# Kernel optimization log

Hardware: AMD Instinct MI355X
Metric: run time of the kernel (lower is better)

The kernel has to match this reference:

```python
import jax, jax.numpy as jnp
import numpy as np

B, N, C = 2, 4096, 256
H = 8          # num heads
D = C // H     # head dim = 32
SR = 2         # spatial reduction ratio
HID = 1024     # mixffn hidden = 4*C
EPS = 1e-5


def layernorm(x, g, b):
    mu = jnp.mean(x, axis=-1, keepdims=True)
    var = jnp.mean(jnp.square(x - mu), axis=-1, keepdims=True)
    return (x - mu) * jax.lax.rsqrt(var + EPS) * g + b


def conv2d(x, w, b, stride, pad, groups=1):
    out = jax.lax.conv_general_dilated(
        x, w, (stride, stride), [(pad, pad), (pad, pad)],
        dimension_numbers=("NCHW", "OIHW", "NCHW"), feature_group_count=groups)
    return out + b[None, :, None, None]


def setup_inputs() -> dict:
    key = jax.random.key(0)
    ks = jax.random.split(key, 20)
    s = lambda k, shape, scale=0.02: jax.random.normal(k, shape, jnp.float32) * scale
    return {
        "x": jax.random.normal(ks[0], (B, N, C), jnp.float32),
        "h": 64, "w": 64,
        "ln1_g": jnp.ones((C,), jnp.float32), "ln1_b": jnp.zeros((C,), jnp.float32),
        "q_w": s(ks[1], (C, C)),
        "kv_w": s(ks[2], (2 * C, C)),
        "sr_w": s(ks[3], (C, C, SR, SR)), "sr_b": jnp.zeros((C,), jnp.float32),
        "srn_g": jnp.ones((C,), jnp.float32), "srn_b": jnp.zeros((C,), jnp.float32),
        "proj_w": s(ks[4], (C, C)), "proj_b": jnp.zeros((C,), jnp.float32),
        "ln2_g": jnp.ones((C,), jnp.float32), "ln2_b": jnp.zeros((C,), jnp.float32),
        "fc1_w": s(ks[5], (HID, C)), "fc1_b": jnp.zeros((HID,), jnp.float32),
        "pe_w": s(ks[6], (HID, 1, 3, 3)), "pe_b": jnp.zeros((HID,), jnp.float32),
        "fc2_w": s(ks[7], (C, HID)), "fc2_b": jnp.zeros((C,), jnp.float32),
    }


def reference(x, h, w, ln1_g, ln1_b, q_w, kv_w, sr_w, sr_b, srn_g, srn_b,
              proj_w, proj_b, ln2_g, ln2_b, fc1_w, fc1_b, pe_w, pe_b, fc2_w, fc2_b):
    b_, n_, c_ = x.shape
    # ---- attention branch ----
    xn = layernorm(x, ln1_g, ln1_b)
    q = jnp.einsum("bnc,oc->bno", xn, q_w).reshape(b_, n_, H, D).transpose(0, 2, 1, 3)  # [B,H,N,D]
    # spatial-reduction of KV
    x_kv = xn.reshape(b_, h, w, c_).transpose(0, 3, 1, 2)              # [B,C,h,w]
    x_kv = conv2d(x_kv, sr_w, sr_b, stride=SR, pad=0)                  # [B,C,h/SR,w/SR]
    nkv = (h // SR) * (w // SR)
    x_kv = x_kv.reshape(b_, c_, nkv).transpose(0, 2, 1)                # [B,Nkv,C]
    x_kv = layernorm(x_kv, srn_g, srn_b)
    kv = jnp.einsum("bnc,oc->bno", x_kv, kv_w).reshape(b_, nkv, 2, H, D)
    k = kv[:, :, 0].transpose(0, 2, 1, 3)                              # [B,H,Nkv,D]
    v = kv[:, :, 1].transpose(0, 2, 1, 3)
    scale = D ** -0.5
    att = jax.nn.softmax(jnp.einsum("bhxd,bhyd->bhxy", q, k) * scale, axis=-1)
    o = jnp.einsum("bhxy,bhyd->bhxd", att, v)                          # [B,H,N,D]
    o = o.transpose(0, 2, 1, 3).reshape(b_, n_, c_)
    o = jnp.einsum("bnc,oc->bno", o, proj_w) + proj_b
    x = x + o
    # ---- Mix-FFN branch ----
    xn2 = layernorm(x, ln2_g, ln2_b)
    xf = xn2.reshape(b_, h, w, c_).transpose(0, 3, 1, 2)               # [B,C,h,w]
    xf = jnp.einsum("bchw,oc->bohw", xf, fc1_w) + fc1_b[None, :, None, None]
    xf = conv2d(xf, pe_w, pe_b, stride=1, pad=1, groups=HID)           # depthwise 3x3
    xf = jax.nn.gelu(xf, approximate=False)
    xf = jnp.einsum("bchw,oc->bohw", xf, fc2_w) + fc2_b[None, :, None, None]
    xf = xf.transpose(0, 2, 3, 1).reshape(b_, n_, c_)
    return x + xf
```

## Files before the change

### kernel.cpp

```cpp
#include <hip/hip_runtime.h>
#include <math.h>

constexpr int BB   = 2;
constexpr int NN   = 4096;
constexpr int CCH  = 256;
constexpr int NH   = 8;
constexpr int HD   = 32;
constexpr int GW   = 64;
constexpr int NKV  = 1024;
constexpr int HIDN = 1024;
constexpr float EPSF = 1e-5f;

typedef short  bf16x8 __attribute__((ext_vector_type(8)));
typedef short  bf16x4 __attribute__((ext_vector_type(4)));
typedef float  f32x4  __attribute__((ext_vector_type(4)));

__device__ __forceinline__ short f2bf(float f) {
    unsigned int u = __float_as_uint(f);
    unsigned int r = (u + 0x7FFFu + ((u >> 16) & 1u)) >> 16;
    return (short)r;
}
__device__ __forceinline__ float bf2f(short s) {
    return __uint_as_float(((unsigned int)(unsigned short)s) << 16);
}
__device__ __forceinline__ unsigned int cvtpk_bf16(float a, float b) {
    unsigned int r;
    asm("v_cvt_pk_bf16_f32 %0, %1, %2" : "=v"(r) : "v"(a), "v"(b));
    return r;
}
__device__ __forceinline__ void gl16(const void* g, void* l) {
    __builtin_amdgcn_global_load_lds(
        (const __attribute__((address_space(1))) void*)g,
        (__attribute__((address_space(3))) void*)l, 16, 0, 0);
}

__global__ __launch_bounds__(256) void prep_kernel(const float* __restrict__ q_w,
                                                   const float* __restrict__ kv_w,
                                                   const float* __restrict__ proj_w,
                                                   const float* __restrict__ fc1_w,
                                                   const float* __restrict__ fc2_w,
                                                   const float* __restrict__ sr_w,
                                                   short* qwb, short* kvwb, short* pjwb,
                                                   short* f1wb, short* f2wb, short* srwb,
                                                   const float* __restrict__ x,
                                                   const float* __restrict__ ln1_g,
                                                   const float* __restrict__ ln1_b,
                                                   short* __restrict__ xn) {
    __shared__ float pa[4], pb[4];
    int t = threadIdx.x;
    if (blockIdx.x < 4096) {
        int i = blockIdx.x * 256 + t;
        if (i < 65536) { qwb[i] = f2bf(q_w[i] * 0.17677669529663687f); return; }
        i -= 65536;
        if (i < 131072) { kvwb[i] = f2bf(kv_w[i]); return; }
        i -= 131072;
        if (i < 65536) { pjwb[i] = f2bf(proj_w[i]); return; }
        i -= 65536;
        if (i < 262144) { f1wb[i] = f2bf(fc1_w[i]); return; }
        i -= 262144;
        if (i < 262144) { f2wb[i] = f2bf(fc2_w[i]); return; }
        i -= 262144;
        {
            int o = i >> 10, rem = i & 1023, c = rem >> 2, q = rem & 3;
            srwb[o * 1024 + q * 256 + c] = f2bf(sr_w[i]);
        }
        return;
    }
    int row = blockIdx.x - 4096;
    float v = x[row * CCH + t];
    float a = v, b = v * v;
#pragma unroll
    for (int off = 32; off > 0; off >>= 1) {
        a += __shfl_xor(a, off);
        b += __shfl_xor(b, off);
    }
    int w = t >> 6;
    if ((t & 63) == 0) { pa[w] = a; pb[w] = b; }
    __syncthreads();
    a = pa[0] + pa[1] + pa[2] + pa[3];
    b = pb[0] + pb[1] + pb[2] + pb[3];
    float mu = a * (1.0f / CCH);
    float var = b * (1.0f / CCH) - mu * mu;
    float rs = rsqrtf(var + EPSF);
    xn[row * CCH + t] = f2bf((v - mu) * rs * ln1_g[t] + ln1_b[t]);
}

template <bool INBF>
__global__ __launch_bounds__(256) void ln_wave(const void* __restrict__ in,
                                               const float* __restrict__ g,
                                               const float* __restrict__ bta,
                                               short* __restrict__ out) {
    int t = threadIdx.x;
    int w = t >> 6, lane = t & 63;
    int row = blockIdx.x * 4 + w;
    float v[4];
    if (INBF) {
        bf16x4 bv = *(const bf16x4*)&((const short*)in)[(size_t)row * CCH + lane * 4];
#pragma unroll
        for (int j = 0; j < 4; j++) v[j] = bf2f(bv[j]);
    } else {
        float4 fv = *(const float4*)&((const float*)in)[(size_t)row * CCH + lane * 4];
        v[0] = fv.x; v[1] = fv.y; v[2] = fv.z; v[3] = fv.w;
    }
    float a = v[0] + v[1] + v[2] + v[3];
    float b = v[0]*v[0] + v[1]*v[1] + v[2]*v[2] + v[3]*v[3];
#pragma unroll
    for (int off = 1; off < 64; off <<= 1) {
        a += __shfl_xor(a, off);
        b += __shfl_xor(b, off);
    }
    float mu = a * (1.0f / CCH);
    float var = b * (1.0f / CCH) - mu * mu;
    float rs = rsqrtf(var + EPSF);
    bf16x4 ov;
#pragma unroll
    for (int j = 0; j < 4; j++)
        ov[j] = f2bf((v[j] - mu) * rs * g[lane * 4 + j] + bta[lane * 4 + j]);
    *(bf16x4*)&out[(size_t)row * CCH + lane * 4] = ov;
}

template <bool OUTB, int RESMODE>
__device__ __forceinline__ void gemm64_body(const short* __restrict__ A,
                                            const short* __restrict__ W,
                                            const float* __restrict__ bias,
                                            const void* __restrict__ res,
                                            void* __restrict__ outp,
                                            int M, int O, int K, int bx, int by,
                                            short (*As0)[64], short (*Ws0)[64],
                                            short (*As1)[64], short (*Ws1)[64]) {
    int t = threadIdx.x;
    int m0 = by * 64, o0 = bx * 64;
    int w = t >> 6, lane = t & 63;
    int wm = (w >> 1) * 32, wn = (w & 1) * 32;
    int fr = lane & 15, fq = lane >> 4;
    int srow = lane >> 3;
    int sg   = (lane & 7) ^ srow;
    f32x4 acc[2][2];
#pragma unroll
    for (int mi = 0; mi < 2; mi++)
#pragma unroll
        for (int ni = 0; ni < 2; ni++)
            acc[mi][ni] = f32x4{0.f, 0.f, 0.f, 0.f};

    auto stage = [&](short (*Asb)[64], short (*Wsb)[64], int k0) {
#pragma unroll
        for (int r = 0; r < 2; r++) {
            int rowA = r * 32 + w * 8 + srow;
            gl16(&A[(size_t)(m0 + rowA) * K + k0 + sg * 8], &Asb[r * 32 + w * 8][0]);
            gl16(&W[(size_t)(o0 + rowA) * K + k0 + sg * 8], &Wsb[r * 32 + w * 8][0]);
        }
    };
    auto compute = [&](short (*Asb)[64], short (*Wsb)[64]) {
#pragma unroll
        for (int half = 0; half < 2; half++) {
            bf16x8 af[2], wf[2];
#pragma unroll
            for (int mi = 0; mi < 2; mi++) {
                int row = wm + mi * 16 + fr;
                af[mi] = *(const bf16x8*)&Asb[row][(((half << 2) | fq) ^ (row & 7)) * 8];
            }
#pragma unroll
            for (int ni = 0; ni < 2; ni++) {
                int row = wn + ni * 16 + fr;
                wf[ni] = *(const bf16x8*)&Wsb[row][(((half << 2) | fq) ^ (row & 7)) * 8];
            }
#pragma unroll
            for (int mi = 0; mi < 2; mi++)
#pragma unroll
                for (int ni = 0; ni < 2; ni++)
                    acc[mi][ni] = __builtin_amdgcn_mfma_f32_16x16x32_bf16(
                        af[mi], wf[ni], acc[mi][ni], 0, 0, 0);
        }
    };

    stage(As0, Ws0, 0);
    __syncthreads();
    for (int k0 = 0; k0 < K; k0 += 128) {
        if (k0 + 64 < K) stage(As1, Ws1, k0 + 64);
        compute(As0, Ws0);
        __syncthreads();
        if (k0 + 128 < K) stage(As0, Ws0, k0 + 128);
        if (k0 + 64 < K) compute(As1, Ws1);
        __syncthreads();
    }
#pragma unroll
    for (int mi = 0; mi < 2; mi++)
#pragma unroll
        for (int ni = 0; ni < 2; ni++)
#pragma unroll
            for (int r = 0; r < 4; r++) {
                int m = m0 + wm + mi * 16 + fq * 4 + r;
                int o = o0 + wn + ni * 16 + fr;
                float v = acc[mi][ni][r];
                if (bias) v += bias[o];
                if (RESMODE == 1) v += ((const float*)res)[(size_t)m * O + o];
                if (RESMODE == 2) v += bf2f(((const short*)res)[(size_t)m * O + o]);
                if (OUTB) ((short*)outp)[(size_t)m * O + o] = f2bf(v);
                else      ((float*)outp)[(size_t)m * O + o] = v;
            }
}

template <bool OUTB, int RESMODE>
__global__ __launch_bounds__(256, 4) void gemm64(const short* __restrict__ A,
                                                 const short* __restrict__ W,
                                                 const float* __restrict__ bias,
                                                 const void* __restrict__ res,
                                                 void* __restrict__ outp,
                                                 int M, int O, int K) {
    __shared__ short As0[64][64], Ws0[64][64];
    __shared__ short As1[64][64], Ws1[64][64];
    gemm64_body<OUTB, RESMODE>(A, W, bias, res, outp, M, O, K,
                               blockIdx.x, blockIdx.y, As0, Ws0, As1, Ws1);
}

__device__ __forceinline__ void sr_body(const short* __restrict__ xn,
                                        const short* __restrict__ Wsr,
                                        const float* __restrict__ sr_b,
                                        float* __restrict__ srtmp, int bx, int by,
                                        short (*As0)[64], short (*As1)[64],
                                        short (*Ws0)[64], short (*Ws1)[64]) {
    int t = threadIdx.x;
    int m0 = by * 32, o0 = bx * 64;
    int w = t >> 6, lane = t & 63;
    int wm = (w >> 1) * 16, wn = (w & 1) * 32;
    int fr = lane & 15, fq = lane >> 4;
    int srow = lane >> 3;
    int sg   = (lane & 7) ^ srow;
    int arow = w * 8 + srow;
    int p = m0 + arow;
    int b = p >> 10, pp = p & 1023, ii = pp >> 5, jj = pp & 31;
    int nbase = ii * 128 + jj * 2;
    size_t xbase = (size_t)(b * NN) * CCH;
    f32x4 acc[2];
    acc[0] = f32x4{0.f, 0.f, 0.f, 0.f};
    acc[1] = f32x4{0.f, 0.f, 0.f, 0.f};

    auto stage = [&](short (*Asb)[64], short (*Wsb)[64], int k0) {
        int q = k0 >> 8, c0 = k0 & 255;
        int n = nbase + (q >> 1) * 64 + (q & 1);
        gl16(&xn[xbase + (size_t)n * CCH + c0 + sg * 8], &Asb[w * 8][0]);
#pragma unroll
        for (int r = 0; r < 2; r++)
            gl16(&Wsr[(size_t)(o0 + r * 32 + w * 8 + srow) * 1024 + k0 + sg * 8],
                 &Wsb[r * 32 + w * 8][0]);
    };
    auto compute = [&](short (*Asb)[64], short (*Wsb)[64]) {
#pragma unroll
        for (int half = 0; half < 2; half++) {
            int cg = (half << 2) | fq;
            int rowa = wm + fr;
            bf16x8 af = *(const bf16x8*)&Asb[rowa][(cg ^ (rowa & 7)) * 8];
            bf16x8 wf[2];
#pragma unroll
            for (int ni = 0; ni < 2; ni++) {
                int row = wn + ni * 16 + fr;
                wf[ni] = *(const bf16x8*)&Wsb[row][(cg ^ (row & 7)) * 8];
            }
#pragma unroll
            for (int ni = 0; ni < 2; ni++)
                acc[ni] = __builtin_amdgcn_mfma_f32_16x16x32_bf16(
                    af, wf[ni], acc[ni], 0, 0, 0);
        }
    };

    stage(As0, Ws0, 0);
    __syncthreads();
    for (int k0 = 0; k0 < 1024; k0 += 128) {
        if (k0 + 64 < 1024) stage(As1, Ws1, k0 + 64);
        compute(As0, Ws0);
        __syncthreads();
        if (k0 + 128 < 1024) stage(As0, Ws0, k0 + 128);
        compute(As1, Ws1);
        __syncthreads();
    }
#pragma unroll
    for (int ni = 0; ni < 2; ni++)
#pragma unroll
        for (int r = 0; r < 4; r++) {
            int m = m0 + wm + fq * 4 + r;
            int o = o0 + wn + ni * 16 + fr;
            srtmp[(size_t)m * CCH + o] = acc[ni][r] + sr_b[o];
        }
}

__global__ __launch_bounds__(256, 4) void qsr_gemm(const short* __restrict__ xn,
                                                   const short* __restrict__ qwb,
                                                   short* __restrict__ qb,
                                                   const short* __restrict__ srwb,
                                                   const float* __restrict__ sr_b,
                                                   float* __restrict__ srtmp) {
    __shared__ short pool[16384];
    int i = blockIdx.x;
    if (i < 512) {
        gemm64_body<true, 0>(xn, qwb, nullptr, nullptr, qb, BB * NN, CCH, CCH,
                             i & 3, i >> 2,
                             (short(*)[64])(pool),
                             (short(*)[64])(pool + 4096),
                             (short(*)[64])(pool + 8192),
                             (short(*)[64])(pool + 12288));
    } else {
        i -= 512;
        sr_body(xn, srwb, sr_b, srtmp, i & 3, i >> 2,
                (short(*)[64])(pool),
                (short(*)[64])(pool + 2048),
                (short(*)[64])(pool + 4096),
                (short(*)[64])(pool + 8192));
    }
}

__global__ __launch_bounds__(256, 2) void gemm_fc1(const short* __restrict__ A,
                                                   const short* __restrict__ W,
                                                   const float* __restrict__ bias,
                                                   short* __restrict__ outp,
                                                   int M, int O, int K) {
    __shared__ short As0[128][64], Ws0[128][64];
    __shared__ short As1[128][64], Ws1[128][64];
    int t = threadIdx.x;
    int m0 = blockIdx.y * 128, o0 = blockIdx.x * 128;
    int w = t >> 6, lane = t & 63;
    int wm = (w >> 1) * 64, wn = (w & 1) * 64;
    int fr = lane & 15, fq = lane >> 4;
    int srow = lane >> 3;
    int sg   = (lane & 7) ^ srow;
    f32x4 acc[4][4];
#pragma unroll
    for (int mi = 0; mi < 4; mi++)
#pragma unroll
        for (int ni = 0; ni < 4; ni++)
            acc[mi][ni] = f32x4{0.f, 0.f, 0.f, 0.f};

    auto stage = [&](short (*Asb)[64], short (*Wsb)[64], int k0) {
#pragma unroll
        for (int r = 0; r < 4; r++) {
            int rowA = r * 32 + w * 8 + srow;
            gl16(&A[(size_t)(m0 + rowA) * K + k0 + sg * 8], &Asb[r * 32 + w * 8][0]);
            gl16(&W[(size_t)(o0 + rowA) * K + k0 + sg * 8], &Wsb[r * 32 + w * 8][0]);
        }
    };
    auto compute = [&](short (*Asb)[64], short (*Wsb)[64]) {
#pragma unroll
        for (int half = 0; half < 2; half++) {
            bf16x8 af[4], wf[4];
#pragma unroll
            for (int mi = 0; mi < 4; mi++) {
                int row = wm + mi * 16 + fr;
                af[mi] = *(const bf16x8*)&Asb[row][(((half << 2) | fq) ^ (row & 7)) * 8];
            }
#pragma unroll
            for (int ni = 0; ni < 4; ni++) {
                int row = wn + ni * 16 + fr;
                wf[ni] = *(const bf16x8*)&Wsb[row][(((half << 2) | fq) ^ (row & 7)) * 8];
            }
#pragma unroll
            for (int mi = 0; mi < 4; mi++)
#pragma unroll
                for (int ni = 0; ni < 4; ni++)
                    acc[mi][ni] = __builtin_amdgcn_mfma_f32_16x16x32_bf16(
                        af[mi], wf[ni], acc[mi][ni], 0, 0, 0);
        }
    };

    stage(As0, Ws0, 0);
    __syncthreads();
    for (int k0 = 0; k0 < K; k0 += 128) {
        if (k0 + 64 < K) stage(As1, Ws1, k0 + 64);
        compute(As0, Ws0);
        __syncthreads();
        if (k0 + 128 < K) stage(As0, Ws0, k0 + 128);
        if (k0 + 64 < K) compute(As1, Ws1);
        __syncthreads();
    }
#pragma unroll
    for (int mi = 0; mi < 4; mi++)
#pragma unroll
        for (int ni = 0; ni < 4; ni++)
#pragma unroll
            for (int r = 0; r < 4; r++) {
                int m = m0 + wm + mi * 16 + fq * 4 + r;
                int o = o0 + wn + ni * 16 + fr;
                outp[(size_t)m * O + o] = f2bf(acc[mi][ni][r] + bias[o]);
            }
}

__global__ __launch_bounds__(256, 4) void kv_gemm(const short* __restrict__ A,
                                                  const short* __restrict__ W,
                                                  short* __restrict__ kvk,
                                                  short* __restrict__ vt) {
    __shared__ short As0[64][64], Ws0[64][64];
    __shared__ short As1[64][64], Ws1[64][64];
    int t = threadIdx.x;
    int m0 = blockIdx.y * 64, o0 = blockIdx.x * 64;
    int w = t >> 6, lane = t & 63;
    int wm = (w >> 1) * 32, wn = (w & 1) * 32;
    int fr = lane & 15, fq = lane >> 4;
    int srow = lane >> 3;
    int sg   = (lane & 7) ^ srow;
    f32x4 acc[2][2];
#pragma unroll
    for (int mi = 0; mi < 2; mi++)
#pragma unroll
        for (int ni = 0; ni < 2; ni++)
            acc[mi][ni] = f32x4{0.f, 0.f, 0.f, 0.f};

    auto stage = [&](short (*Asb)[64], short (*Wsb)[64], int k0) {
#pragma unroll
        for (int r = 0; r < 2; r++) {
            int rowA = r * 32 + w * 8 + srow;
            gl16(&A[(size_t)(m0 + rowA) * CCH + k0 + sg * 8], &Asb[r * 32 + w * 8][0]);
            gl16(&W[(size_t)(o0 + rowA) * CCH + k0 + sg * 8], &Wsb[r * 32 + w * 8][0]);
        }
    };
    auto compute = [&](short (*Asb)[64], short (*Wsb)[64]) {
#pragma unroll
        for (int half = 0; half < 2; half++) {
            bf16x8 af[2], wf[2];
#pragma unroll
            for (int mi = 0; mi < 2; mi++) {
                int row = wm + mi * 16 + fr;
                af[mi] = *(const bf16x8*)&Asb[row][(((half << 2) | fq) ^ (row & 7)) * 8];
            }
#pragma unroll
            for (int ni = 0; ni < 2; ni++) {
                int row = wn + ni * 16 + fr;
                wf[ni] = *(const bf16x8*)&Wsb[row][(((half << 2) | fq) ^ (row & 7)) * 8];
            }
#pragma unroll
            for (int mi = 0; mi < 2; mi++)
#pragma unroll
                for (int ni = 0; ni < 2; ni++)
                    acc[mi][ni] = __builtin_amdgcn_mfma_f32_16x16x32_bf16(
                        af[mi], wf[ni], acc[mi][ni], 0, 0, 0);
        }
    };

    stage(As0, Ws0, 0);
    __syncthreads();
    stage(As1, Ws1, 64);
    compute(As0, Ws0);
    __syncthreads();
    stage(As0, Ws0, 128);
    compute(As1, Ws1);
    __syncthreads();
    stage(As1, Ws1, 192);
    compute(As0, Ws0);
    __syncthreads();
    compute(As1, Ws1);

#pragma unroll
    for (int mi = 0; mi < 2; mi++)
#pragma unroll
        for (int ni = 0; ni < 2; ni++) {
            int o = o0 + wn + ni * 16 + fr;
            int mbase = m0 + wm + mi * 16 + fq * 4;
            if (o < 256) {
#pragma unroll
                for (int r = 0; r < 4; r++)
                    kvk[(size_t)(mbase + r) * 256 + o] = f2bf(acc[mi][ni][r]);
            } else {
                int h = (o - 256) >> 5, d = (o - 256) & 31;
                int b = mbase >> 10, y0 = mbase & 1023;
                size_t rowbase = ((size_t)((b * NH + h) * HD) + d) * NKV + (y0 >> 6) * 64;
                int y4 = y0 & 63;
#pragma unroll
                for (int r = 0; r < 4; r++) {
                    int y64 = y4 + r;
                    int s = (y64 & 15) * 4 + (y64 >> 4);
                    vt[rowbase + s] = f2bf(acc[mi][ni][r]);
                }
            }
        }
}

__global__ __launch_bounds__(256, 3) void attn_mfma(const short* __restrict__ qb,
                                                    const short* __restrict__ kvk,
                                                    const short* __restrict__ vt,
                                                    short* __restrict__ o) {
    int blk = blockIdx.x;
    int qt = blk & 31; int hh = (blk >> 5) & 7; int b = blk >> 8;
    int t = threadIdx.x; int w = t >> 6; int lane = t & 63;
    int fr = lane & 15, fq = lane >> 4;
    __shared__ short Ks0[128][32], Ks1[128][32];
    __shared__ short Vt0[64][64],  Vt1[64][64];
    __shared__ short Ps[4][2][16][64];
    int n0 = qt * 128 + w * 16;
    bf16x8 qa[2];
#pragma unroll
    for (int mi = 0; mi < 2; mi++)
        qa[mi] = *(const bf16x8*)&qb[((size_t)(b * NN) + n0 + mi * 64 + fr) * CCH + hh * HD + fq * 8];
    f32x4 oacc[2][2];
    float lst[2][4];
#pragma unroll
    for (int mi = 0; mi < 2; mi++) {
#pragma unroll
        for (int nd = 0; nd < 2; nd++) oacc[mi][nd] = f32x4{0.f, 0.f, 0.f, 0.f};
#pragma unroll
        for (int r = 0; r < 4; r++) lst[mi][r] = 0.f;
    }

    int srowK = lane >> 2;
    int sgK   = (lane & 3) ^ (srowK & 3);
    int srowV = lane >> 3;
    int sgV   = (lane & 7) ^ srowV;

    auto stageKV = [&](short (*Ksb)[32], short (*Vtb)[64], int y0) {
#pragma unroll
        for (int r2 = 0; r2 < 2; r2++) {
            int rowK = r2 * 64 + w * 16 + srowK;
            gl16(&kvk[((size_t)(b * NKV) + y0 + rowK) * 256 + hh * HD + sgK * 8],
                 &Ksb[r2 * 64 + w * 16][0]);
        }
#pragma unroll
        for (int r3 = 0; r3 < 2; r3++) {
            int d = w * 8 + srowV;
            gl16(&vt[((size_t)((b * NH + hh) * HD) + d) * NKV + y0 + r3 * 64 + sgV * 8],
                 &Vtb[r3 * 32 + w * 8][0]);
        }
    };
    auto tile = [&](short (*Ksb)[32], short (*Vtb)[64]) {
#pragma unroll
        for (int h2 = 0; h2 < 2; h2++) {
#pragma unroll
            for (int mi = 0; mi < 2; mi++) {
                f32x4 s[4];
                __builtin_amdgcn_s_setprio(1);
#pragma unroll
                for (int ni = 0; ni < 4; ni++) {
                    int rowk = h2 * 64 + ni * 16 + fr;
                    bf16x8 kb = *(const bf16x8*)&Ksb[rowk][(fq ^ (fr & 3)) * 8];
                    s[ni] = __builtin_amdgcn_mfma_f32_16x16x32_bf16(
                        qa[mi], kb, f32x4{0.f, 0.f, 0.f, 0.f}, 0, 0, 0);
                }
                __builtin_amdgcn_s_setprio(0);
#pragma unroll
                for (int r = 0; r < 4; r++) {
                    int row = fq * 4 + r;
                    float p0 = __expf(fminf(s[0][r], 30.f));
                    float p1 = __expf(fminf(s[1][r], 30.f));
                    float p2 = __expf(fminf(s[2][r], 30.f));
                    float p3 = __expf(fminf(s[3][r], 30.f));
                    lst[mi][r] += (p0 + p1) + (p2 + p3);
                    unsigned int w0 = cvtpk_bf16(p0, p1);
                    unsigned int w1 = cvtpk_bf16(p2, p3);
                    int gp = (fr >> 1) ^ (row & 7);
                    *(uint2*)&Ps[w][mi][row][gp * 8 + (fr & 1) * 4] = make_uint2(w0, w1);
                }
                __builtin_amdgcn_s_setprio(1);
#pragma unroll
                for (int ks = 0; ks < 2; ks++) {
                    int gk = ks * 4 + fq;
                    bf16x8 pa = *(const bf16x8*)&Ps[w][mi][fr][(gk ^ (fr & 7)) * 8];
#pragma unroll
                    for (int nd = 0; nd < 2; nd++) {
                        int rowv = nd * 16 + fr;
                        bf16x8 vb = *(const bf16x8*)&Vtb[h2 * 32 + rowv][(gk ^ (rowv & 7)) * 8];
                        oacc[mi][nd] = __builtin_amdgcn_mfma_f32_16x16x32_bf16(
                            pa, vb, oacc[mi][nd], 0, 0, 0);
                    }
                }
                __builtin_amdgcn_s_setprio(0);
            }
        }
    };

    stageKV(Ks0, Vt0, 0);
    __syncthreads();
    for (int y0 = 0; y0 < NKV; y0 += 256) {
        if (y0 + 128 < NKV) stageKV(Ks1, Vt1, y0 + 128);
        tile(Ks0, Vt0);
        __syncthreads();
        if (y0 + 256 < NKV) stageKV(Ks0, Vt0, y0 + 256);
        tile(Ks1, Vt1);
        __syncthreads();
    }
#pragma unroll
    for (int mi = 0; mi < 2; mi++)
#pragma unroll
        for (int r = 0; r < 4; r++) {
            float ls = lst[mi][r];
#pragma unroll
            for (int off = 1; off < 16; off <<= 1)
                ls += __shfl_xor(ls, off);
            float inv = 1.f / ls;
            int row = n0 + mi * 64 + fq * 4 + r;
#pragma unroll
            for (int nd = 0; nd < 2; nd++)
                o[((size_t)(b * NN) + row) * CCH + hh * HD + nd * 16 + fr] =
                    f2bf(oacc[mi][nd][r] * inv);
        }
}

__global__ __launch_bounds__(256, 2) void dwconv_gelu(const short* __restrict__ xf,
                                                      const float* __restrict__ pe_w,
                                                      const float* __restrict__ pe_b,
                                                      short* __restrict__ out) {
    int blk = blockIdx.x;
    int cg = blk & 15, sp = (blk >> 4) & 15, b = blk >> 8;
    int r0 = (sp >> 2) * 16, c0 = (sp & 3) * 16;
    int ch0 = cg * 64;
    int t = threadIdx.x;
    __shared__ short tile[18][18][64];
    for (int idx = t; idx < 18 * 18 * 8; idx += 256) {
        int pix = idx >> 3, part = idx & 7;
        int row = pix / 18, col = pix - row * 18;
        int gr = r0 + row - 1, gc = c0 + col - 1;
        bf16x8 v = {0, 0, 0, 0, 0, 0, 0, 0};
        if (gr >= 0 && gr < 64 && gc >= 0 && gc < 64)
            v = *(const bf16x8*)&xf[((size_t)(b * NN) + gr * GW + gc) * HIDN + ch0 + part * 8];
        *(bf16x8*)&tile[row][col][part * 8] = v;
    }
    __syncthreads();
    int cl = t & 63, sg = t >> 6;
    int ch = ch0 + cl;
    float wv[9];
#pragma unroll
    for (int k = 0; k < 9; k++) wv[k] = pe_w[ch * 9 + k];
    float bias = pe_b[ch];
#pragma unroll
    for (int q = 0; q < 4; q++) {
        int lr = sg * 4 + q;
        float cA[3], cB[3], cC[3];
#pragma unroll
        for (int ki = 0; ki < 3; ki++) {
            cA[ki] = bf2f(tile[lr + ki][0][cl]);
            cB[ki] = bf2f(tile[lr + ki][1][cl]);
        }
        for (int cc = 0; cc < 16; cc++) {
#pragma unroll
            for (int ki = 0; ki < 3; ki++) cC[ki] = bf2f(tile[lr + ki][cc + 2][cl]);
            float acc = bias;
#pragma unroll
            for (int ki = 0; ki < 3; ki++)
                acc += cA[ki] * wv[ki * 3] + cB[ki] * wv[ki * 3 + 1] + cC[ki] * wv[ki * 3 + 2];
            float z = 0.7978845608f * (acc + 0.044715f * acc * acc * acc);
            float e = __expf(-2.f * fabsf(z));
            float th = (1.f - e) / (1.f + e);
            th = (z < 0.f) ? -th : th;
            float gg = 0.5f * acc * (1.f + th);
            out[((size_t)(b * NN) + (r0 + lr) * GW + c0 + cc) * HIDN + ch] = f2bf(gg);
#pragma unroll
            for (int ki = 0; ki < 3; ki++) { cA[ki] = cB[ki]; cB[ki] = cC[ki]; }
        }
    }
}

extern "C" void kernel_launch(void* const* d_in, const int* in_sizes, int n_in,
                              void* d_out, int out_size, void* d_ws, size_t ws_size,
                              hipStream_t stream) {
    const float* x      = (const float*)d_in[0];
    const float* ln1_g  = (const float*)d_in[3];
    const float* ln1_b  = (const float*)d_in[4];
    const float* q_w    = (const float*)d_in[5];
    const float* kv_w   = (const float*)d_in[6];
    const float* sr_w   = (const float*)d_in[7];
    const float* sr_b   = (const float*)d_in[8];
    const float* srn_g  = (const float*)d_in[9];
    const float* srn_b  = (const float*)d_in[10];
    const float* proj_w = (const float*)d_in[11];
    const float* proj_b = (const float*)d_in[12];
    const float* ln2_g  = (const float*)d_in[13];
    const float* ln2_b  = (const float*)d_in[14];
    const float* fc1_w  = (const float*)d_in[15];
    const float* fc1_b  = (const float*)d_in[16];
    const float* pe_w   = (const float*)d_in[17];
    const float* pe_b   = (const float*)d_in[18];
    const float* fc2_w  = (const float*)d_in[19];
    const float* fc2_b  = (const float*)d_in[20];
    float* out = (float*)d_out;

    char* base = (char*)d_ws;
    short* xn    = (short*)(base);
    short* qb    = (short*)(base + (4ull  << 20));
    float* srtmp = (float*)(base + (12ull << 20));
    short* xkvn  = (short*)(base + (14ull << 20));
    short* kvk   = (short*)(base + (15ull << 20));
    short* vtb   = (short*)(base + (17ull << 20));
    short* obf   = (short*)(base + (18ull << 20));
    short* x1    = (short*)(base + (22ull << 20));
    short* xf1   = (short*)(base + (30ull << 20));
    short* xf2g  = (short*)(base + (46ull << 20));
    short* qwb   = (short*)(base + (62ull << 20));
    short* kvwb  = qwb  + 65536;
    short* pjwb  = kvwb + 131072;
    short* f1wb  = pjwb + 65536;
    short* f2wb  = f1wb + 262144;
    short* srwb  = f2wb + 262144;

    prep_kernel<<<4096 + BB * NN, 256, 0, stream>>>(q_w, kv_w, proj_w, fc1_w, fc2_w, sr_w,
                                                    qwb, kvwb, pjwb, f1wb, f2wb, srwb,
                                                    x, ln1_g, ln1_b, xn);
    qsr_gemm<<<768, 256, 0, stream>>>(xn, qwb, qb, srwb, sr_b, srtmp);
    ln_wave<false><<<BB * NKV / 4, 256, 0, stream>>>(srtmp, srn_g, srn_b, xkvn);
    {
        dim3 g(512 / 64, (BB * NKV) / 64);
        kv_gemm<<<g, 256, 0, stream>>>(xkvn, kvwb, kvk, vtb);
    }
    attn_mfma<<<BB * NH * (NN / 128), 256, 0, stream>>>(qb, kvk, vtb, obf);
    {
        dim3 g(CCH / 64, (BB * NN) / 64);
        gemm64<true, 1><<<g, 256, 0, stream>>>(obf, pjwb, proj_b, x, x1, BB * NN, CCH, CCH);
    }
    ln_wave<true><<<BB * NN / 4, 256, 0, stream>>>(x1, ln2_g, ln2_b, xn);
    {
        dim3 g(HIDN / 128, (BB * NN) / 128);
        gemm_fc1<<<g, 256, 0, stream>>>(xn, f1wb, fc1_b, xf1, BB * NN, HIDN, CCH);
    }
    dwconv_gelu<<<BB * 256, 256, 0, stream>>>(xf1, pe_w, pe_b, xf2g);
    {
        dim3 g(CCH / 64, (BB * NN) / 64);
        gemm64<false, 2><<<g, 256, 0, stream>>>(xf2g, f2wb, fc2_b, x1, out, BB * NN, CCH, HIDN);
    }
}
```

Baseline: 115.6 us.

## Fuse layernorms into KV and fc1 GEMMs via full-K shared A tiles

The two standalone layernorm kernels, one after the spatial-reduction conv and one before fc1, are removed. Each consuming GEMM now normalizes its 64-row A tile across the full 256-channel K dimension into padded shared memory, then streams only the weight tiles through a double buffer. This saves two launches and the round trip of the normalized activations through global memory. In exchange, each column block recomputes the layernorm for its rows, the fc1 tile shape changes from 128x128 to 64x128, and shared memory per block grows.

```diff
diff --git a/kernel.cpp b/kernel.cpp
--- a/kernel.cpp
+++ b/kernel.cpp
@@ -85,40 +85,6 @@
     xn[row * CCH + t] = f2bf((v - mu) * rs * ln1_g[t] + ln1_b[t]);
 }
 
-template <bool INBF>
-__global__ __launch_bounds__(256) void ln_wave(const void* __restrict__ in,
-                                               const float* __restrict__ g,
-                                               const float* __restrict__ bta,
-                                               short* __restrict__ out) {
-    int t = threadIdx.x;
-    int w = t >> 6, lane = t & 63;
-    int row = blockIdx.x * 4 + w;
-    float v[4];
-    if (INBF) {
-        bf16x4 bv = *(const bf16x4*)&((const short*)in)[(size_t)row * CCH + lane * 4];
-#pragma unroll
-        for (int j = 0; j < 4; j++) v[j] = bf2f(bv[j]);
-    } else {
-        float4 fv = *(const float4*)&((const float*)in)[(size_t)row * CCH + lane * 4];
-        v[0] = fv.x; v[1] = fv.y; v[2] = fv.z; v[3] = fv.w;
-    }
-    float a = v[0] + v[1] + v[2] + v[3];
-    float b = v[0]*v[0] + v[1]*v[1] + v[2]*v[2] + v[3]*v[3];
-#pragma unroll
-    for (int off = 1; off < 64; off <<= 1) {
-        a += __shfl_xor(a, off);
-        b += __shfl_xor(b, off);
-    }
-    float mu = a * (1.0f / CCH);
-    float var = b * (1.0f / CCH) - mu * mu;
-    float rs = rsqrtf(var + EPSF);
-    bf16x4 ov;
-#pragma unroll
-    for (int j = 0; j < 4; j++)
-        ov[j] = f2bf((v[j] - mu) * rs * g[lane * 4 + j] + bta[lane * 4 + j]);
-    *(bf16x4*)&out[(size_t)row * CCH + lane * 4] = ov;
-}
-
 template <bool OUTB, int RESMODE>
 __device__ __forceinline__ void gemm64_body(const short* __restrict__ A,
                                             const short* __restrict__ W,
@@ -308,86 +274,14 @@
     }
 }
 
-__global__ __launch_bounds__(256, 2) void gemm_fc1(const short* __restrict__ A,
-                                                   const short* __restrict__ W,
-                                                   const float* __restrict__ bias,
-                                                   short* __restrict__ outp,
-                                                   int M, int O, int K) {
-    __shared__ short As0[128][64], Ws0[128][64];
-    __shared__ short As1[128][64], Ws1[128][64];
-    int t = threadIdx.x;
-    int m0 = blockIdx.y * 128, o0 = blockIdx.x * 128;
-    int w = t >> 6, lane = t & 63;
-    int wm = (w >> 1) * 64, wn = (w & 1) * 64;
-    int fr = lane & 15, fq = lane >> 4;
-    int srow = lane >> 3;
-    int sg   = (lane & 7) ^ srow;
-    f32x4 acc[4][4];
-#pragma unroll
-    for (int mi = 0; mi < 4; mi++)
-#pragma unroll
-        for (int ni = 0; ni < 4; ni++)
-            acc[mi][ni] = f32x4{0.f, 0.f, 0.f, 0.f};
-
-    auto stage = [&](short (*Asb)[64], short (*Wsb)[64], int k0) {
-#pragma unroll
-        for (int r = 0; r < 4; r++) {
-            int rowA = r * 32 + w * 8 + srow;
-            gl16(&A[(size_t)(m0 + rowA) * K + k0 + sg * 8], &Asb[r * 32 + w * 8][0]);
-            gl16(&W[(size_t)(o0 + rowA) * K + k0 + sg * 8], &Wsb[r * 32 + w * 8][0]);
-        }
-    };
-    auto compute = [&](short (*Asb)[64], short (*Wsb)[64]) {
-#pragma unroll
-        for (int half = 0; half < 2; half++) {
-            bf16x8 af[4], wf[4];
-#pragma unroll
-            for (int mi = 0; mi < 4; mi++) {
-                int row = wm + mi * 16 + fr;
-                af[mi] = *(const bf16x8*)&Asb[row][(((half << 2) | fq) ^ (row & 7)) * 8];
-            }
-#pragma unroll
-            for (int ni = 0; ni < 4; ni++) {
-                int row = wn + ni * 16 + fr;
-                wf[ni] = *(const bf16x8*)&Wsb[row][(((half << 2) | fq) ^ (row & 7)) * 8];
-            }
-#pragma unroll
-            for (int mi = 0; mi < 4; mi++)
-#pragma unroll
-                for (int ni = 0; ni < 4; ni++)
-                    acc[mi][ni] = __builtin_amdgcn_mfma_f32_16x16x32_bf16(
-                        af[mi], wf[ni], acc[mi][ni], 0, 0, 0);
-        }
-    };
-
-    stage(As0, Ws0, 0);
-    __syncthreads();
-    for (int k0 = 0; k0 < K; k0 += 128) {
-        if (k0 + 64 < K) stage(As1, Ws1, k0 + 64);
-        compute(As0, Ws0);
-        __syncthreads();
-        if (k0 + 128 < K) stage(As0, Ws0, k0 + 128);
-        if (k0 + 64 < K) compute(As1, Ws1);
-        __syncthreads();
-    }
-#pragma unroll
-    for (int mi = 0; mi < 4; mi++)
-#pragma unroll
-        for (int ni = 0; ni < 4; ni++)
-#pragma unroll
-            for (int r = 0; r < 4; r++) {
-                int m = m0 + wm + mi * 16 + fq * 4 + r;
-                int o = o0 + wn + ni * 16 + fr;
-                outp[(size_t)m * O + o] = f2bf(acc[mi][ni][r] + bias[o]);
-            }
-}
-
-__global__ __launch_bounds__(256, 4) void kv_gemm(const short* __restrict__ A,
-                                                  const short* __restrict__ W,
-                                                  short* __restrict__ kvk,
-                                                  short* __restrict__ vt) {
-    __shared__ short As0[64][64], Ws0[64][64];
-    __shared__ short As1[64][64], Ws1[64][64];
+__global__ __launch_bounds__(256, 3) void kvln_gemm(const float* __restrict__ srtmp,
+                                                    const float* __restrict__ srn_g,
+                                                    const float* __restrict__ srn_b,
+                                                    const short* __restrict__ W,
+                                                    short* __restrict__ kvk,
+                                                    short* __restrict__ vt) {
+    __shared__ short Als[64][280];
+    __shared__ short Ws0[64][64], Ws1[64][64];
     int t = threadIdx.x;
     int m0 = blockIdx.y * 64, o0 = blockIdx.x * 64;
     int w = t >> 6, lane = t & 63;
@@ -395,34 +289,77 @@
     int fr = lane & 15, fq = lane >> 4;
     int srow = lane >> 3;
     int sg   = (lane & 7) ^ srow;
+    {
+        int cl = lane & 15, rq = lane >> 4;
+        float4 gg0 = *(const float4*)&srn_g[cl * 16];
+        float4 gg1 = *(const float4*)&srn_g[cl * 16 + 4];
+        float4 gg2 = *(const float4*)&srn_g[cl * 16 + 8];
+        float4 gg3 = *(const float4*)&srn_g[cl * 16 + 12];
+        float4 bb0 = *(const float4*)&srn_b[cl * 16];
+        float4 bb1 = *(const float4*)&srn_b[cl * 16 + 4];
+        float4 bb2 = *(const float4*)&srn_b[cl * 16 + 8];
+        float4 bb3 = *(const float4*)&srn_b[cl * 16 + 12];
+#pragma unroll
+        for (int pass = 0; pass < 4; pass++) {
+            int row = w * 16 + pass * 4 + rq;
+            const float* src = &srtmp[(size_t)(m0 + row) * CCH + cl * 16];
+            float4 v0 = *(const float4*)&src[0];
+            float4 v1 = *(const float4*)&src[4];
+            float4 v2 = *(const float4*)&src[8];
+            float4 v3 = *(const float4*)&src[12];
+            float a = (v0.x + v0.y + v0.z + v0.w) + (v1.x + v1.y + v1.z + v1.w)
+                    + (v2.x + v2.y + v2.z + v2.w) + (v3.x + v3.y + v3.z + v3.w);
+            float b = (v0.x*v0.x + v0.y*v0.y + v0.z*v0.z + v0.w*v0.w)
+                    + (v1.x*v1.x + v1.y*v1.y + v1.z*v1.z + v1.w*v1.w)
+                    + (v2.x*v2.x + v2.y*v2.y + v2.z*v2.z + v2.w*v2.w)
+                    + (v3.x*v3.x + v3.y*v3.y + v3.z*v3.z + v3.w*v3.w);
+#pragma unroll
+            for (int off = 1; off < 16; off <<= 1) {
+                a += __shfl_xor(a, off);
+                b += __shfl_xor(b, off);
+            }
+            float mu = a * (1.0f / CCH);
+            float var = b * (1.0f / CCH) - mu * mu;
+            float rs = rsqrtf(var + EPSF);
+            bf16x4 o0v, o1v, o2v, o3v;
+            o0v[0]=f2bf((v0.x-mu)*rs*gg0.x+bb0.x); o0v[1]=f2bf((v0.y-mu)*rs*gg0.y+bb0.y);
+            o0v[2]=f2bf((v0.z-mu)*rs*gg0.z+bb0.z); o0v[3]=f2bf((v0.w-mu)*rs*gg0.w+bb0.w);
+            o1v[0]=f2bf((v1.x-mu)*rs*gg1.x+bb1.x); o1v[1]=f2bf((v1.y-mu)*rs*gg1.y+bb1.y);
+            o1v[2]=f2bf((v1.z-mu)*rs*gg1.z+bb1.z); o1v[3]=f2bf((v1.w-mu)*rs*gg1.w+bb1.w);
+            o2v[0]=f2bf((v2.x-mu)*rs*gg2.x+bb2.x); o2v[1]=f2bf((v2.y-mu)*rs*gg2.y+bb2.y);
+            o2v[2]=f2bf((v2.z-mu)*rs*gg2.z+bb2.z); o2v[3]=f2bf((v2.w-mu)*rs*gg2.w+bb2.w);
+            o3v[0]=f2bf((v3.x-mu)*rs*gg3.x+bb3.x); o3v[1]=f2bf((v3.y-mu)*rs*gg3.y+bb3.y);
+            o3v[2]=f2bf((v3.z-mu)*rs*gg3.z+bb3.z); o3v[3]=f2bf((v3.w-mu)*rs*gg3.w+bb3.w);
+            *(bf16x4*)&Als[row][cl * 16]      = o0v;
+            *(bf16x4*)&Als[row][cl * 16 + 4]  = o1v;
+            *(bf16x4*)&Als[row][cl * 16 + 8]  = o2v;
+            *(bf16x4*)&Als[row][cl * 16 + 12] = o3v;
+        }
+    }
     f32x4 acc[2][2];
 #pragma unroll
     for (int mi = 0; mi < 2; mi++)
 #pragma unroll
         for (int ni = 0; ni < 2; ni++)
             acc[mi][ni] = f32x4{0.f, 0.f, 0.f, 0.f};
-
-    auto stage = [&](short (*Asb)[64], short (*Wsb)[64], int k0) {
-#pragma unroll
-        for (int r = 0; r < 2; r++) {
-            int rowA = r * 32 + w * 8 + srow;
-            gl16(&A[(size_t)(m0 + rowA) * CCH + k0 + sg * 8], &Asb[r * 32 + w * 8][0]);
-            gl16(&W[(size_t)(o0 + rowA) * CCH + k0 + sg * 8], &Wsb[r * 32 + w * 8][0]);
-        }
-    };
-    auto compute = [&](short (*Asb)[64], short (*Wsb)[64]) {
+    auto stageW = [&](short (*Wsb)[64], int k0) {
+#pragma unroll
+        for (int r = 0; r < 2; r++)
+            gl16(&W[(size_t)(o0 + r * 32 + w * 8 + srow) * CCH + k0 + sg * 8],
+                 &Wsb[r * 32 + w * 8][0]);
+    };
+    auto compute = [&](int k0, short (*Wsb)[64]) {
 #pragma unroll
         for (int half = 0; half < 2; half++) {
+            int cg = (half << 2) | fq;
             bf16x8 af[2], wf[2];
 #pragma unroll
-            for (int mi = 0; mi < 2; mi++) {
-                int row = wm + mi * 16 + fr;
-                af[mi] = *(const bf16x8*)&Asb[row][(((half << 2) | fq) ^ (row & 7)) * 8];
-            }
+            for (int mi = 0; mi < 2; mi++)
+                af[mi] = *(const bf16x8*)&Als[wm + mi * 16 + fr][k0 + cg * 8];
 #pragma unroll
             for (int ni = 0; ni < 2; ni++) {
                 int row = wn + ni * 16 + fr;
-                wf[ni] = *(const bf16x8*)&Wsb[row][(((half << 2) | fq) ^ (row & 7)) * 8];
+                wf[ni] = *(const bf16x8*)&Wsb[row][(cg ^ (row & 7)) * 8];
             }
 #pragma unroll
             for (int mi = 0; mi < 2; mi++)
@@ -432,20 +369,18 @@
                         af[mi], wf[ni], acc[mi][ni], 0, 0, 0);
         }
     };
-
-    stage(As0, Ws0, 0);
-    __syncthreads();
-    stage(As1, Ws1, 64);
-    compute(As0, Ws0);
-    __syncthreads();
-    stage(As0, Ws0, 128);
-    compute(As1, Ws1);
-    __syncthreads();
-    stage(As1, Ws1, 192);
-    compute(As0, Ws0);
-    __syncthreads();
-    compute(As1, Ws1);
-
+    stageW(Ws0, 0);
+    __syncthreads();
+    stageW(Ws1, 64);
+    compute(0, Ws0);
+    __syncthreads();
+    stageW(Ws0, 128);
+    compute(64, Ws1);
+    __syncthreads();
+    stageW(Ws1, 192);
+    compute(128, Ws0);
+    __syncthreads();
+    compute(192, Ws1);
 #pragma unroll
     for (int mi = 0; mi < 2; mi++)
 #pragma unroll
@@ -469,6 +404,122 @@
                 }
             }
         }
+}
+
+__global__ __launch_bounds__(256, 2) void fc1ln_gemm(const short* __restrict__ x1,
+                                                     const float* __restrict__ ln2_g,
+                                                     const float* __restrict__ ln2_b,
+                                                     const short* __restrict__ W,
+                                                     const float* __restrict__ bias,
+                                                     short* __restrict__ outp) {
+    __shared__ short Als[64][280];
+    __shared__ short Ws0[128][64], Ws1[128][64];
+    int t = threadIdx.x;
+    int m0 = blockIdx.y * 64, o0 = blockIdx.x * 128;
+    int w = t >> 6, lane = t & 63;
+    int wm = (w >> 1) * 32, wn = (w & 1) * 64;
+    int fr = lane & 15, fq = lane >> 4;
+    int srow = lane >> 3;
+    int sg   = (lane & 7) ^ srow;
+    {
+        int cl = lane & 15, rq = lane >> 4;
+        float4 gg0 = *(const float4*)&ln2_g[cl * 16];
+        float4 gg1 = *(const float4*)&ln2_g[cl * 16 + 4];
+        float4 gg2 = *(const float4*)&ln2_g[cl * 16 + 8];
+        float4 gg3 = *(const float4*)&ln2_g[cl * 16 + 12];
+        float4 bb0 = *(const float4*)&ln2_b[cl * 16];
+        float4 bb1 = *(const float4*)&ln2_b[cl * 16 + 4];
+        float4 bb2 = *(const float4*)&ln2_b[cl * 16 + 8];
+        float4 bb3 = *(const float4*)&ln2_b[cl * 16 + 12];
+#pragma unroll
+        for (int pass = 0; pass < 4; pass++) {
+            int row = w * 16 + pass * 4 + rq;
+            const short* src = &x1[(size_t)(m0 + row) * CCH + cl * 16];
+            bf16x8 u0 = *(const bf16x8*)&src[0];
+            bf16x8 u1 = *(const bf16x8*)&src[8];
+            float v[16];
+#pragma unroll
+            for (int j = 0; j < 8; j++) { v[j] = bf2f(u0[j]); v[8 + j] = bf2f(u1[j]); }
+            float a = 0.f, b = 0.f;
+#pragma unroll
+            for (int j = 0; j < 16; j++) { a += v[j]; b += v[j] * v[j]; }
+#pragma unroll
+            for (int off = 1; off < 16; off <<= 1) {
+                a += __shfl_xor(a, off);
+                b += __shfl_xor(b, off);
+            }
+            float mu = a * (1.0f / CCH);
+            float var = b * (1.0f / CCH) - mu * mu;
+            float rs = rsqrtf(var + EPSF);
+            float g4[16] = {gg0.x, gg0.y, gg0.z, gg0.w, gg1.x, gg1.y, gg1.z, gg1.w,
+                            gg2.x, gg2.y, gg2.z, gg2.w, gg3.x, gg3.y, gg3.z, gg3.w};
+            float b4[16] = {bb0.x, bb0.y, bb0.z, bb0.w, bb1.x, bb1.y, bb1.z, bb1.w,
+                            bb2.x, bb2.y, bb2.z, bb2.w, bb3.x, bb3.y, bb3.z, bb3.w};
+            bf16x8 w0, w1;
+#pragma unroll
+            for (int j = 0; j < 8; j++) {
+                w0[j] = f2bf((v[j] - mu) * rs * g4[j] + b4[j]);
+                w1[j] = f2bf((v[8 + j] - mu) * rs * g4[8 + j] + b4[8 + j]);
+            }
+            *(bf16x8*)&Als[row][cl * 16]     = w0;
+            *(bf16x8*)&Als[row][cl * 16 + 8] = w1;
+        }
+    }
+    f32x4 acc[2][4];
+#pragma unroll
+    for (int mi = 0; mi < 2; mi++)
+#pragma unroll
+        for (int ni = 0; ni < 4; ni++)
+            acc[mi][ni] = f32x4{0.f, 0.f, 0.f, 0.f};
+    auto stageW = [&](short (*Wsb)[64], int k0) {
+#pragma unroll
+        for (int r = 0; r < 4; r++)
+            gl16(&W[(size_t)(o0 + r * 32 + w * 8 + srow) * CCH + k0 + sg * 8],
+                 &Wsb[r * 32 + w * 8][0]);
+    };
+    auto compute = [&](int k0, short (*Wsb)[64]) {
+#pragma unroll
+        for (int half = 0; half < 2; half++) {
+            int cg = (half << 2) | fq;
+            bf16x8 af[2], wf[4];
+#pragma unroll
+            for (int mi = 0; mi < 2; mi++)
+                af[mi] = *(const bf16x8*)&Als[wm + mi * 16 + fr][k0 + cg * 8];
+#pragma unroll
+            for (int ni = 0; ni < 4; ni++) {
+                int row = wn + ni * 16 + fr;
+                wf[ni] = *(const bf16x8*)&Wsb[row][(cg ^ (row & 7)) * 8];
+            }
+#pragma unroll
+            for (int mi = 0; mi < 2; mi++)
+#pragma unroll
+                for (int ni = 0; ni < 4; ni++)
+                    acc[mi][ni] = __builtin_amdgcn_mfma_f32_16x16x32_bf16(
+                        af[mi], wf[ni], acc[mi][ni], 0, 0, 0);
+        }
+    };
+    stageW(Ws0, 0);
+    __syncthreads();
+    stageW(Ws1, 64);
+    compute(0, Ws0);
+    __syncthreads();
+    stageW(Ws0, 128);
+    compute(64, Ws1);
+    __syncthreads();
+    stageW(Ws1, 192);
+    compute(128, Ws0);
+    __syncthreads();
+    compute(192, Ws1);
+#pragma unroll
+    for (int mi = 0; mi < 2; mi++)
+#pragma unroll
+        for (int ni = 0; ni < 4; ni++)
+#pragma unroll
+            for (int r = 0; r < 4; r++) {
+                int m = m0 + wm + mi * 16 + fq * 4 + r;
+                int o = o0 + wn + ni * 16 + fr;
+                outp[(size_t)m * HIDN + o] = f2bf(acc[mi][ni][r] + bias[o]);
+            }
 }
 
 __global__ __launch_bounds__(256, 3) void attn_mfma(const short* __restrict__ qb,
@@ -671,7 +722,6 @@
     short* xn    = (short*)(base);
     short* qb    = (short*)(base + (4ull  << 20));
     float* srtmp = (float*)(base + (12ull << 20));
-    short* xkvn  = (short*)(base + (14ull << 20));
     short* kvk   = (short*)(base + (15ull << 20));
     short* vtb   = (short*)(base + (17ull << 20));
     short* obf   = (short*)(base + (18ull << 20));
@@ -689,20 +739,18 @@
                                                     qwb, kvwb, pjwb, f1wb, f2wb, srwb,
                                                     x, ln1_g, ln1_b, xn);
     qsr_gemm<<<768, 256, 0, stream>>>(xn, qwb, qb, srwb, sr_b, srtmp);
-    ln_wave<false><<<BB * NKV / 4, 256, 0, stream>>>(srtmp, srn_g, srn_b, xkvn);
     {
         dim3 g(512 / 64, (BB * NKV) / 64);
-        kv_gemm<<<g, 256, 0, stream>>>(xkvn, kvwb, kvk, vtb);
+        kvln_gemm<<<g, 256, 0, stream>>>(srtmp, srn_g, srn_b, kvwb, kvk, vtb);
     }
     attn_mfma<<<BB * NH * (NN / 128), 256, 0, stream>>>(qb, kvk, vtb, obf);
     {
         dim3 g(CCH / 64, (BB * NN) / 64);
         gemm64<true, 1><<<g, 256, 0, stream>>>(obf, pjwb, proj_b, x, x1, BB * NN, CCH, CCH);
     }
-    ln_wave<true><<<BB * NN / 4, 256, 0, stream>>>(x1, ln2_g, ln2_b, xn);
     {
-        dim3 g(HIDN / 128, (BB * NN) / 128);
-        gemm_fc1<<<g, 256, 0, stream>>>(xn, f1wb, fc1_b, xf1, BB * NN, HIDN, CCH);
+        dim3 g(HIDN / 128, (BB * NN) / 64);
+        fc1ln_gemm<<<g, 256, 0, stream>>>(x1, ln2_g, ln2_b, f1wb, fc1_b, xf1);
     }
     dwconv_gelu<<<BB * 256, 256, 0, stream>>>(xf1, pe_w, pe_b, xf2g);
     {
```

New measurement: 121.3 us. 4.9% more time.
